# Kernel optimization log

Measured on AMD Instinct MI355X. Metric: run time of the kernel, lower is better.

## Reference

```python
import jax, jax.numpy as jnp
import numpy as np

BITS = 4
QMAX = (1 << BITS) - 1      # 15
QHALF = 1 << (BITS - 1)     # 8
B, S = 4, 2048
IN, OUT, FP = 4096, 4096, 256
INT = IN - FP


def setup_inputs() -> dict:
    key = jax.random.key(0)
    k0, k1, k2, k3 = jax.random.split(key, 4)
    x = jax.random.normal(k0, (B, S, IN), dtype=jnp.float16)
    # disjoint outlier / int feature index sets (QUIK splits columns by outlier-ness)
    perm = np.random.default_rng(0).permutation(IN)
    fp_indices = jnp.sort(jnp.asarray(perm[:FP], dtype=jnp.int32))
    int_indices = jnp.sort(jnp.asarray(perm[FP:], dtype=jnp.int32))
    # unpacked int4 weight values in [-8, 7] (torch stores these packed 2-per-uint8)
    int_weight = jax.random.randint(k1, (OUT, INT), -QHALF, QHALF, dtype=jnp.int8)
    weights_scales = (jax.random.uniform(k2, (OUT, 1), dtype=jnp.float32) * 0.01 + 1e-3).astype(jnp.float16)
    fp_weight = (jax.random.normal(k3, (OUT, FP), dtype=jnp.float32) * 0.02).astype(jnp.float16)
    bias = jnp.zeros((OUT,), dtype=jnp.float16)
    # reduced_w[j] = w_scale[j] * sum_k int_weight[j, k]  (precomputed zero-point correction)
    reduced_w = (weights_scales.astype(jnp.float32)[:, 0] * jnp.sum(int_weight.astype(jnp.float32), axis=1)).reshape(1, OUT).astype(jnp.float16)
    return {"x": x, "int_weight": int_weight, "fp_weight": fp_weight, "bias": bias,
            "weights_scales": weights_scales, "reduced_w": reduced_w,
            "int_indices": int_indices, "fp_indices": fp_indices}


def reference(x, int_weight, fp_weight, bias, weights_scales, reduced_w, int_indices, fp_indices):
    b, s, in_feat = x.shape
    xf = x.reshape(-1, in_feat)                       # [N, in] tokens
    int_x = xf[:, int_indices].astype(jnp.float32)    # [N, INT]
    fp_x = xf[:, fp_indices].astype(jnp.float32)      # [N, FP] outliers stay fp16-precision
    # asymmetric per-token quantization (quik.asymmetric.quantize)
    mn = jnp.min(int_x, axis=1, keepdims=True)
    mx = jnp.max(int_x, axis=1, keepdims=True)
    scale = jnp.maximum((mx - mn) / QMAX, 1e-8)       # [N,1]
    q = (jnp.clip(jnp.round((int_x - mn) / scale), 0, QMAX) - QHALF).astype(jnp.int8)  # signed int4 in [-8,7]
    zero = scale * QHALF + mn                         # [N,1] shifted zero point
    # int4 GEMM (quik.matmul.int4Matmul), int32 accumulate
    int_res = jnp.einsum('nk,ok->no', q, int_weight, preferred_element_type=jnp.int32)
    # fp outlier branch fused with bias (F.linear)
    fp_res = fp_x @ fp_weight.astype(jnp.float32).T + bias.astype(jnp.float32)[None, :]
    # quik.asymmetric.dequantize: q*scale_x*scale_w + zero_x*reduced_w + fp_result
    out = (int_res.astype(jnp.float32) * scale * weights_scales.astype(jnp.float32)[:, 0][None, :]
           + zero * reduced_w.astype(jnp.float32) + fp_res)
    return out.astype(jnp.float16).reshape(b, s, -1)
```

## Files before the change

### kernel.cpp

```cpp
#include <hip/hip_runtime.h>
#include <hip/hip_bf16.h>
#include <stdint.h>

#define N_TOK 8192
#define IN_F  4096
#define OUT_F 4096
#define FP_F  256
#define INT_F 3840
#define PROW  1920

typedef int    v4i   __attribute__((ext_vector_type(4)));
typedef int    v16i  __attribute__((ext_vector_type(16)));
typedef float  v16f  __attribute__((ext_vector_type(16)));
typedef __bf16 bf16x8 __attribute__((ext_vector_type(8)));

#define WS_QP   0u
#define WS_WP   15728640u
#define WS_FPX  23592960u
#define WS_WFP  27787264u
#define WS_F1   29884416u
#define WS_F2   29917184u
#define WS_F3   29949952u
#define WS_NEED 29982720u


__global__ __launch_bounds__(256) void zero_out_kernel(uint4* __restrict__ o) {
  o[(size_t)blockIdx.x * 256 + threadIdx.x] = uint4{0, 0, 0, 0};
}

__global__ __launch_bounds__(256, 4) void prep_kernel(
    const float* __restrict__ x,
    const int* __restrict__ int_idx, const int* __restrict__ fp_idx,
    const int* __restrict__ int_w, const float* __restrict__ fp_w,
    uint8_t* __restrict__ qp, uint8_t* __restrict__ wp,
    __hip_bfloat16* __restrict__ fpx, __hip_bfloat16* __restrict__ wfp,
    float* __restrict__ f1, float* __restrict__ f2, float* __restrict__ f3) {
  __shared__ uint2 qb[960];

  int tid = threadIdx.x;
  int blk = blockIdx.x;

  if (blk >= 2048) {
    int pb = blk - 2048;
    if (pb < 7680) {
      int t = pb * 256 + tid;
      int r = t / 480, u = t % 480;
      int g = u >> 1, h = u & 1;
      const int* src = int_w + (size_t)r * INT_F + g * 16 + h * 4;
      int4 lo = *(const int4*)src;
      int4 hi = *(const int4*)(src + 8);
      uint32_t o = (uint32_t)((lo.x + 8) & 15) | (uint32_t)((hi.x + 8) & 15) << 4 |
                   (uint32_t)((lo.y + 8) & 15) << 8 | (uint32_t)((hi.y + 8) & 15) << 12 |
                   (uint32_t)((lo.z + 8) & 15) << 16 | (uint32_t)((hi.z + 8) & 15) << 20 |
                   (uint32_t)((lo.w + 8) & 15) << 24 | (uint32_t)((hi.w + 8) & 15) << 28;
      int gs = (g & ~7) | ((g & 7) ^ ((r >> 1) & 7));
      ((uint32_t*)wp)[(size_t)r * 480 + gs * 2 + h] = o;
    } else {
      int t = (pb - 7680) * 256 + tid;
      int i = t * 4;
      int r = i >> 8, c = i & 255;
      float4 v = *(const float4*)(fp_w + i);
      __hip_bfloat16 b[4] = {__float2bfloat16(v.x), __float2bfloat16(v.y),
                             __float2bfloat16(v.z), __float2bfloat16(v.w)};
      int cs = (c & ~0x18) | (((((c) >> 3) & 3) ^ ((r >> 1) & 3)) << 3);
      *(uint2*)(wfp + (size_t)r * 256 + cs) = *(const uint2*)b;
    }
    return;
  }

  int wave = tid >> 6, l = tid & 63;
  int n = blk * 4 + wave;
  const float* xr = x + (size_t)n * IN_F;

  float v[60];
  float lmn = 1e30f, lmx = -1e30f;
#pragma unroll
  for (int k = 0; k < 60; k++) {
    v[k] = xr[int_idx[l + 64 * k]];
    lmn = fminf(lmn, v[k]);
    lmx = fmaxf(lmx, v[k]);
  }
  {
    int sw2 = (n >> 1) & 3;
#pragma unroll
    for (int j = 0; j < 4; j++) {
      int c = l + 64 * j;
      int cs = (c & ~0x18) | ((((c >> 3) & 3) ^ sw2) << 3);
      fpx[(size_t)n * FP_F + cs] = __float2bfloat16(xr[fp_idx[c]]);
    }
  }

#pragma unroll
  for (int off = 32; off > 0; off >>= 1) {
    lmn = fminf(lmn, __shfl_xor(lmn, off, 64));
    lmx = fmaxf(lmx, __shfl_xor(lmx, off, 64));
  }
  float mn = lmn;
  float sc = fmaxf((lmx - mn) / 15.0f, 1e-8f);
  float inv = 1.0f / sc;
  if (l == 0) { f1[n] = sc; f3[n] = mn; }

  uint8_t* qbw = (uint8_t*)qb + wave * 1920;
  int swq = (n >> 1) & 7;
  float lsum = 0.0f;
#pragma unroll
  for (int k = 0; k < 60; k++) {
    float c = fminf(fmaxf(rintf((v[k] - mn) * inv), 0.0f), 15.0f);
    lsum += c;
    float ch = __shfl_down(c, 8, 64);
    if ((l & 15) < 8) {
      int G = (l >> 4) + 4 * k;
      int pos = ((G & ~7) | ((G & 7) ^ swq)) * 8 + (l & 7);
      qbw[pos] = (uint8_t)((uint32_t)c | ((uint32_t)ch << 4));
    }
  }
#pragma unroll
  for (int off = 32; off > 0; off >>= 1) lsum += __shfl_xor(lsum, off, 64);
  if (l == 0) f2[n] = -8.0f * lsum * sc;

  const uint2* qbu = qb + wave * 240;
#pragma unroll
  for (int r = 0; r < 4; r++) {
    int i = l + 64 * r;
    if (i < 240) *(uint2*)(qp + (size_t)n * PROW + i * 8) = qbu[i];
  }
}

__device__ inline v4i unpack_nib(uint2 u) {
  v4i r;
  r[0] = (int)(u.x & 0x0F0F0F0Fu);
  r[1] = (int)(u.y & 0x0F0F0F0Fu);
  r[2] = (int)((u.x >> 4) & 0x0F0F0F0Fu);
  r[3] = (int)((u.y >> 4) & 0x0F0F0F0Fu);
  return r;
}

__device__ __forceinline__ void gl16(const void* g, void* l) {
  __builtin_amdgcn_global_load_lds(
      (const __attribute__((address_space(1))) void*)g,
      (__attribute__((address_space(3))) void*)l, 16, 0, 0);
}

__global__ __launch_bounds__(256, 4) void gemm_kernel(
    const uint8_t* __restrict__ qp, const uint8_t* __restrict__ wp,
    const __hip_bfloat16* __restrict__ fpx, const __hip_bfloat16* __restrict__ wfp,
    const float* __restrict__ f1, const float* __restrict__ f2,
    const float* __restrict__ f3,
    const float* __restrict__ wscale, const float* __restrict__ reduced,
    const float* __restrict__ bias, float* __restrict__ out) {
  __shared__ int4 lds4[2048];
  int8_t* lds = (int8_t*)lds4;

  int tid = threadIdx.x;
  int wave = tid >> 6, lane = tid & 63;
  int wm = wave >> 1, wn = wave & 1;
  int blk = blockIdx.x;
  int tileM = ((blk & 7) << 3) | ((blk >> 3) & 7);
  int tileN = blk >> 6;
  int n0 = tileM * 128, o0 = tileN * 128;

  union { v16i i; v16f f; } acc[2][2];
#pragma unroll
  for (int mi = 0; mi < 2; mi++)
#pragma unroll
    for (int ni = 0; ni < 2; ni++)
#pragma unroll
      for (int e = 0; e < 16; e++) acc[mi][ni].i[e] = 0;

  int m = lane & 31, kg = lane >> 5;

  int row0 = tid >> 2, q16 = (tid & 3) * 16;
  int l0 = tid * 16, l1 = 4096 + tid * 16;
  const uint8_t* gA0 = qp + (size_t)(n0 + row0) * PROW + q16;
  const uint8_t* gA1 = qp + (size_t)(n0 + 64 + row0) * PROW + q16;
  const uint8_t* gB0 = wp + (size_t)(o0 + row0) * PROW + q16;
  const uint8_t* gB1 = wp + (size_t)(o0 + 64 + row0) * PROW + q16;

#define STAGE_INT(buf, kt) do {                                  \
    gl16(gA0 + (kt) * 64, lds + (buf) * 16384 + l0);             \
    gl16(gA1 + (kt) * 64, lds + (buf) * 16384 + l1);             \
    gl16(gB0 + (kt) * 64, lds + (buf) * 16384 + 8192 + l0);      \
    gl16(gB1 + (kt) * 64, lds + (buf) * 16384 + 8192 + l1);      \
  } while (0)

  auto compute_int = [&](const int8_t* lb) {
#pragma unroll
    for (int ks = 0; ks < 4; ks++) {
      int s8 = ks * 2 + kg;
      v4i a[2], b[2];
#pragma unroll
      for (int mi = 0; mi < 2; mi++) {
        int row = wm * 64 + mi * 32 + m;
        a[mi] = unpack_nib(*(const uint2*)&lb[row * 64 + ((s8 ^ ((row >> 1) & 7)) * 8)]);
      }
#pragma unroll
      for (int ni = 0; ni < 2; ni++) {
        int row = wn * 64 + ni * 32 + m;
        b[ni] = unpack_nib(*(const uint2*)&lb[8192 + row * 64 + ((s8 ^ ((row >> 1) & 7)) * 8)]);
      }
#pragma unroll
      for (int mi = 0; mi < 2; mi++)
#pragma unroll
        for (int ni = 0; ni < 2; ni++)
          acc[mi][ni].i = __builtin_amdgcn_mfma_i32_32x32x32_i8(
              a[mi], b[ni], acc[mi][ni].i, 0, 0, 0);
    }
  };

  STAGE_INT(0, 0);
#pragma unroll 1
  for (int kt = 0; kt < 30; kt += 2) {
    STAGE_INT(1, kt + 1);
    asm volatile("s_waitcnt vmcnt(4)" ::: "memory");
    __builtin_amdgcn_s_barrier();
    compute_int(lds);
    __builtin_amdgcn_s_barrier();
    if (kt + 2 < 30) {
      STAGE_INT(0, kt + 2);
      asm volatile("s_waitcnt vmcnt(4)" ::: "memory");
    } else {
      asm volatile("s_waitcnt vmcnt(0)" ::: "memory");
    }
    __builtin_amdgcn_s_barrier();
    compute_int(lds + 16384);
    __builtin_amdgcn_s_barrier();
  }

  const uint8_t* fxb = (const uint8_t*)fpx;
  const uint8_t* fwb = (const uint8_t*)wfp;
  const uint8_t* gFA0 = fxb + (size_t)(n0 + row0) * 512 + q16;
  const uint8_t* gFA1 = fxb + (size_t)(n0 + 64 + row0) * 512 + q16;
  const uint8_t* gFB0 = fwb + (size_t)(o0 + row0) * 512 + q16;
  const uint8_t* gFB1 = fwb + (size_t)(o0 + 64 + row0) * 512 + q16;

#define STAGE_BF(buf, kr) do {                                   \
    gl16(gFA0 + (kr) * 64, lds + (buf) * 16384 + l0);            \
    gl16(gFA1 + (kr) * 64, lds + (buf) * 16384 + l1);            \
    gl16(gFB0 + (kr) * 64, lds + (buf) * 16384 + 8192 + l0);     \
    gl16(gFB1 + (kr) * 64, lds + (buf) * 16384 + 8192 + l1);     \
  } while (0)

  STAGE_BF(0, 0);

  int col = lane & 31, rb4 = (lane >> 5) * 4;
  float cws[2], crw[2], cbs[2];
#pragma unroll
  for (int ni = 0; ni < 2; ni++) {
    int o = o0 + wn * 64 + ni * 32 + col;
    cws[ni] = wscale[o]; crw[ni] = reduced[o]; cbs[ni] = bias[o];
  }
#pragma unroll
  for (int mi = 0; mi < 2; mi++) {
#pragma unroll
    for (int reg = 0; reg < 16; reg++) {
      int row = (reg & 3) + 8 * (reg >> 2) + rb4;
      int n = n0 + wm * 64 + mi * 32 + row;
      float a1 = f1[n], a2 = f2[n], a3 = f3[n];
      float d0 = (float)acc[mi][0].i[reg];
      float d1 = (float)acc[mi][1].i[reg];
      acc[mi][0].f[reg] = (d0 * a1 + a2) * cws[0] + a3 * crw[0] + cbs[0];
      acc[mi][1].f[reg] = (d1 * a1 + a2) * cws[1] + a3 * crw[1] + cbs[1];
    }
  }

  auto compute_bf = [&](const int8_t* lb) {
#pragma unroll
    for (int kstep = 0; kstep < 2; kstep++) {
      int s16 = kstep * 2 + kg;
      bf16x8 a[2], b[2];
#pragma unroll
      for (int mi = 0; mi < 2; mi++) {
        int row = wm * 64 + mi * 32 + m;
        a[mi] = *(const bf16x8*)&lb[row * 64 + ((s16 ^ ((row >> 1) & 3)) * 16)];
      }
#pragma unroll
      for (int ni = 0; ni < 2; ni++) {
        int row = wn * 64 + ni * 32 + m;
        b[ni] = *(const bf16x8*)&lb[8192 + row * 64 + ((s16 ^ ((row >> 1) & 3)) * 16)];
      }
#pragma unroll
      for (int mi = 0; mi < 2; mi++)
#pragma unroll
        for (int ni = 0; ni < 2; ni++)
          acc[mi][ni].f = __builtin_amdgcn_mfma_f32_32x32x16_bf16(
              a[mi], b[ni], acc[mi][ni].f, 0, 0, 0);
    }
  };

#pragma unroll 1
  for (int kr = 0; kr < 8; kr += 2) {
    STAGE_BF(1, kr + 1);
    asm volatile("s_waitcnt vmcnt(4)" ::: "memory");
    __builtin_amdgcn_s_barrier();
    compute_bf(lds);
    __builtin_amdgcn_s_barrier();
    if (kr + 2 < 8) {
      STAGE_BF(0, kr + 2);
      asm volatile("s_waitcnt vmcnt(4)" ::: "memory");
    } else {
      asm volatile("s_waitcnt vmcnt(0)" ::: "memory");
    }
    __builtin_amdgcn_s_barrier();
    compute_bf(lds + 16384);
    __builtin_amdgcn_s_barrier();
  }
#undef STAGE_INT
#undef STAGE_BF

#pragma unroll
  for (int mi = 0; mi < 2; mi++) {
#pragma unroll
    for (int ni = 0; ni < 2; ni++) {
      int o = o0 + wn * 64 + ni * 32 + col;
#pragma unroll
      for (int reg = 0; reg < 16; reg++) {
        int row = (reg & 3) + 8 * (reg >> 2) + rb4;
        int n = n0 + wm * 64 + mi * 32 + row;
        out[(size_t)n * OUT_F + o] = acc[mi][ni].f[reg];
      }
    }
  }
}

extern "C" void kernel_launch(void* const* d_in, const int* in_sizes, int n_in,
                              void* d_out, int out_size, void* d_ws, size_t ws_size,
                              hipStream_t stream) {
  const float* x     = (const float*)d_in[0];
  const int*   int_w = (const int*)d_in[1];
  const float* fp_w  = (const float*)d_in[2];
  const float* bias  = (const float*)d_in[3];
  const float* wsc   = (const float*)d_in[4];
  const float* red   = (const float*)d_in[5];
  const int*   iidx  = (const int*)d_in[6];
  const int*   fidx  = (const int*)d_in[7];
  float*       out   = (float*)d_out;

  if (ws_size < (size_t)WS_NEED) {
    zero_out_kernel<<<out_size / 1024, 256, 0, stream>>>((uint4*)d_out);
    return;
  }

  uint8_t* ws = (uint8_t*)d_ws;
  uint8_t*        qp  = ws + WS_QP;
  uint8_t*        wpk = ws + WS_WP;
  __hip_bfloat16* fpx = (__hip_bfloat16*)(ws + WS_FPX);
  __hip_bfloat16* wfp = (__hip_bfloat16*)(ws + WS_WFP);
  float*          f1  = (float*)(ws + WS_F1);
  float*          f2  = (float*)(ws + WS_F2);
  float*          f3  = (float*)(ws + WS_F3);

  prep_kernel<<<2048 + 7680 + 1024, 256, 0, stream>>>(
      x, iidx, fidx, int_w, fp_w, qp, wpk, fpx, wfp, f1, f2, f3);
  gemm_kernel<<<(N_TOK / 128) * (OUT_F / 128), 256, 0, stream>>>(
      qp, wpk, fpx, wfp, f1, f2, f3, wsc, red, bias, out);
}
```

Before: 409.3 us.

## Store weights pre-unpacked as int8 in k-major slabs to skip nibble unpacking

The prep kernel now writes the int4 weights as one nibble per byte, already in the layout the MFMA B operand expects, arranged in k-slab-major blocks. The GEMM then loads B fragments straight from LDS with no unpack instructions. The cost is double the weight bytes in memory and in LDS per stage (24 KB per buffer), more global loads per stage, and launch bounds lowered to 3 blocks per CU. The BF16 tail stage now uses an explicit byte offset into the same LDS and adds a full wait and barrier before its loop.

```diff
diff --git a/kernel.cpp b/kernel.cpp
--- a/kernel.cpp
+++ b/kernel.cpp
@@ -16,12 +16,12 @@
 
 #define WS_QP   0u
 #define WS_WP   15728640u
-#define WS_FPX  23592960u
-#define WS_WFP  27787264u
-#define WS_F1   29884416u
-#define WS_F2   29917184u
-#define WS_F3   29949952u
-#define WS_NEED 29982720u
+#define WS_FPX  31457280u
+#define WS_WFP  35651584u
+#define WS_F1   37748736u
+#define WS_F2   37781504u
+#define WS_F3   37814272u
+#define WS_NEED 37847040u
 
 
 __global__ __launch_bounds__(256) void zero_out_kernel(uint4* __restrict__ o) {
@@ -42,21 +42,18 @@
 
   if (blk >= 2048) {
     int pb = blk - 2048;
-    if (pb < 7680) {
+    if (pb < 15360) {
       int t = pb * 256 + tid;
-      int r = t / 480, u = t % 480;
-      int g = u >> 1, h = u & 1;
-      const int* src = int_w + (size_t)r * INT_F + g * 16 + h * 4;
-      int4 lo = *(const int4*)src;
-      int4 hi = *(const int4*)(src + 8);
-      uint32_t o = (uint32_t)((lo.x + 8) & 15) | (uint32_t)((hi.x + 8) & 15) << 4 |
-                   (uint32_t)((lo.y + 8) & 15) << 8 | (uint32_t)((hi.y + 8) & 15) << 12 |
-                   (uint32_t)((lo.z + 8) & 15) << 16 | (uint32_t)((hi.z + 8) & 15) << 20 |
-                   (uint32_t)((lo.w + 8) & 15) << 24 | (uint32_t)((hi.w + 8) & 15) << 28;
-      int gs = (g & ~7) | ((g & 7) ^ ((r >> 1) & 7));
-      ((uint32_t*)wp)[(size_t)r * 480 + gs * 2 + h] = o;
+      int r = t / 960, u = t % 960;
+      const int* src = int_w + (size_t)r * INT_F + u * 4;
+      int4 w4 = *(const int4*)src;
+      uint32_t pk = (uint32_t)((w4.x + 8) & 15) |
+                    (uint32_t)((w4.y + 8) & 15) << 8 |
+                    (uint32_t)((w4.z + 8) & 15) << 16 |
+                    (uint32_t)((w4.w + 8) & 15) << 24;
+      *(uint32_t*)(wp + (size_t)(u >> 2) * 65536 + (size_t)r * 16 + (u & 3) * 4) = pk;
     } else {
-      int t = (pb - 7680) * 256 + tid;
+      int t = (pb - 15360) * 256 + tid;
       int i = t * 4;
       int r = i >> 8, c = i & 255;
       float4 v = *(const float4*)(fp_w + i);
@@ -141,14 +138,14 @@
       (__attribute__((address_space(3))) void*)l, 16, 0, 0);
 }
 
-__global__ __launch_bounds__(256, 4) void gemm_kernel(
+__global__ __launch_bounds__(256, 3) void gemm_kernel(
     const uint8_t* __restrict__ qp, const uint8_t* __restrict__ wp,
     const __hip_bfloat16* __restrict__ fpx, const __hip_bfloat16* __restrict__ wfp,
     const float* __restrict__ f1, const float* __restrict__ f2,
     const float* __restrict__ f3,
     const float* __restrict__ wscale, const float* __restrict__ reduced,
     const float* __restrict__ bias, float* __restrict__ out) {
-  __shared__ int4 lds4[2048];
+  __shared__ int4 lds4[3072];
   int8_t* lds = (int8_t*)lds4;
 
   int tid = threadIdx.x;
@@ -173,14 +170,18 @@
   int l0 = tid * 16, l1 = 4096 + tid * 16;
   const uint8_t* gA0 = qp + (size_t)(n0 + row0) * PROW + q16;
   const uint8_t* gA1 = qp + (size_t)(n0 + 64 + row0) * PROW + q16;
-  const uint8_t* gB0 = wp + (size_t)(o0 + row0) * PROW + q16;
-  const uint8_t* gB1 = wp + (size_t)(o0 + 64 + row0) * PROW + q16;
-
-#define STAGE_INT(buf, kt) do {                                  \
-    gl16(gA0 + (kt) * 64, lds + (buf) * 16384 + l0);             \
-    gl16(gA1 + (kt) * 64, lds + (buf) * 16384 + l1);             \
-    gl16(gB0 + (kt) * 64, lds + (buf) * 16384 + 8192 + l0);      \
-    gl16(gB1 + (kt) * 64, lds + (buf) * 16384 + 8192 + l1);      \
+
+  int rB = tid & 127, sB = tid >> 7;
+  const uint8_t* gBk = wp + (size_t)sB * 65536 + (size_t)(o0 + rB) * 16;
+  int lB = 8192 + sB * 2048 + rB * 16;
+
+#define STAGE_INT(buf, kt) do {                                          \
+    gl16(gA0 + (kt) * 64, lds + (buf) * 24576 + l0);                     \
+    gl16(gA1 + (kt) * 64, lds + (buf) * 24576 + l1);                     \
+    gl16(gBk + (size_t)(kt) * 524288,          lds + (buf) * 24576 + lB);          \
+    gl16(gBk + (size_t)(kt) * 524288 + 131072, lds + (buf) * 24576 + lB + 4096);   \
+    gl16(gBk + (size_t)(kt) * 524288 + 262144, lds + (buf) * 24576 + lB + 8192);   \
+    gl16(gBk + (size_t)(kt) * 524288 + 393216, lds + (buf) * 24576 + lB + 12288);  \
   } while (0)
 
   auto compute_int = [&](const int8_t* lb) {
@@ -196,7 +197,7 @@
 #pragma unroll
       for (int ni = 0; ni < 2; ni++) {
         int row = wn * 64 + ni * 32 + m;
-        b[ni] = unpack_nib(*(const uint2*)&lb[8192 + row * 64 + ((s8 ^ ((row >> 1) & 7)) * 8)]);
+        b[ni] = *(const v4i*)&lb[8192 + s8 * 2048 + row * 16];
       }
 #pragma unroll
       for (int mi = 0; mi < 2; mi++)
@@ -211,18 +212,18 @@
 #pragma unroll 1
   for (int kt = 0; kt < 30; kt += 2) {
     STAGE_INT(1, kt + 1);
-    asm volatile("s_waitcnt vmcnt(4)" ::: "memory");
+    asm volatile("s_waitcnt vmcnt(6)" ::: "memory");
     __builtin_amdgcn_s_barrier();
     compute_int(lds);
     __builtin_amdgcn_s_barrier();
     if (kt + 2 < 30) {
       STAGE_INT(0, kt + 2);
-      asm volatile("s_waitcnt vmcnt(4)" ::: "memory");
+      asm volatile("s_waitcnt vmcnt(6)" ::: "memory");
     } else {
       asm volatile("s_waitcnt vmcnt(0)" ::: "memory");
     }
     __builtin_amdgcn_s_barrier();
-    compute_int(lds + 16384);
+    compute_int(lds + 24576);
     __builtin_amdgcn_s_barrier();
   }
 
@@ -234,10 +235,10 @@
   const uint8_t* gFB1 = fwb + (size_t)(o0 + 64 + row0) * 512 + q16;
 
 #define STAGE_BF(buf, kr) do {                                   \
-    gl16(gFA0 + (kr) * 64, lds + (buf) * 16384 + l0);            \
-    gl16(gFA1 + (kr) * 64, lds + (buf) * 16384 + l1);            \
-    gl16(gFB0 + (kr) * 64, lds + (buf) * 16384 + 8192 + l0);     \
-    gl16(gFB1 + (kr) * 64, lds + (buf) * 16384 + 8192 + l1);     \
+    gl16(gFA0 + (kr) * 64, lds + (buf) + l0);                    \
+    gl16(gFA1 + (kr) * 64, lds + (buf) + l1);                    \
+    gl16(gFB0 + (kr) * 64, lds + (buf) + 8192 + l0);             \
+    gl16(gFB1 + (kr) * 64, lds + (buf) + 8192 + l1);             \
   } while (0)
 
   STAGE_BF(0, 0);
@@ -262,6 +263,8 @@
       acc[mi][1].f[reg] = (d1 * a1 + a2) * cws[1] + a3 * crw[1] + cbs[1];
     }
   }
+  asm volatile("s_waitcnt vmcnt(0)" ::: "memory");
+  __builtin_amdgcn_s_barrier();
 
   auto compute_bf = [&](const int8_t* lb) {
 #pragma unroll
@@ -289,7 +292,7 @@
 
 #pragma unroll 1
   for (int kr = 0; kr < 8; kr += 2) {
-    STAGE_BF(1, kr + 1);
+    STAGE_BF(16384, kr + 1);
     asm volatile("s_waitcnt vmcnt(4)" ::: "memory");
     __builtin_amdgcn_s_barrier();
     compute_bf(lds);
@@ -349,7 +352,7 @@
   float*          f2  = (float*)(ws + WS_F2);
   float*          f3  = (float*)(ws + WS_F3);
 
-  prep_kernel<<<2048 + 7680 + 1024, 256, 0, stream>>>(
+  prep_kernel<<<2048 + 15360 + 1024, 256, 0, stream>>>(
       x, iidx, fidx, int_w, fp_w, qp, wpk, fpx, wfp, f1, f2, f3);
   gemm_kernel<<<(N_TOK / 128) * (OUT_F / 128), 256, 0, stream>>>(
       qp, wpk, fpx, wfp, f1, f2, f3, wsc, red, bias, out);
```

After: 413.7 us. About the same (+1.1%).
